# Kernel optimization log

Hardware: AMD Instinct MI355X
Metric: run time of the kernel (lower is better)

## Reference

```python
import jax, jax.numpy as jnp
import numpy as np


def setup_inputs() -> dict:
    key = jax.random.key(0)
    k1, k2, k3, k4 = jax.random.split(key, 4)
    b, c, h, w = 4, 256, 64, 64
    Fq_l = jax.random.normal(k1, (b, c, h, w), dtype=jnp.float32)
    Fp_l = jax.random.normal(k2, (b, c, h, w), dtype=jnp.float32)
    # 1x1 conv: weight [out=c//2, in=c], bias [c//2]
    W = jax.random.normal(k3, (c // 2, c), dtype=jnp.float32) * (1.0 / np.sqrt(c))
    bias = jax.random.normal(k4, (c // 2,), dtype=jnp.float32) * 0.01
    return {"Fq_l": Fq_l, "Fp_l": Fp_l, "W": W, "bias": bias}


def reference(Fq_l, Fp_l, W, bias):
    b, c, h, w = Fq_l.shape
    hw = h * w
    # 1x1 conv == per-pixel linear projection
    q = jnp.einsum('oc,bchw->bohw', W, Fq_l) + bias[None, :, None, None]
    p = jnp.einsum('oc,bchw->bohw', W, Fp_l) + bias[None, :, None, None]
    qf = q.reshape(b, -1, hw)  # [b, c/2, hw]
    pf = p.reshape(b, -1, hw)
    qf = qf / jnp.linalg.norm(qf, axis=1, keepdims=True)
    pf = pf / jnp.linalg.norm(pf, axis=1, keepdims=True)
    # cosine similarity, [b, hw, hw]
    sim = jnp.einsum('bcn,bcm->bnm', qf, pf)
    idx = jnp.argmax(sim, axis=-1)  # [b, hw]
    Fp_flat = Fp_l.reshape(b, c, hw)
    aligned = jnp.take_along_axis(Fp_flat, idx[:, None, :], axis=2)  # [b, c, hw]
    return aligned.reshape(b, c, h, w)
```

## Files before the change

### kernel.cpp

```cpp
#include <hip/hip_runtime.h>

#define HW 4096
#define BCAP 1024u
#define OCAP 65536u

typedef short bf16x8 __attribute__((ext_vector_type(8)));
typedef float f32x16 __attribute__((ext_vector_type(16)));

__device__ __forceinline__ ushort f2bf_rne(float f) {
    unsigned u = __float_as_uint(f);
    return (ushort)((u + 0x7FFFu + ((u >> 16) & 1u)) >> 16);
}

__global__ __launch_bounds__(256) void init_kernel(
    unsigned long long* __restrict__ best, unsigned* __restrict__ bcnt,
    unsigned* __restrict__ ocnt)
{
    int i = blockIdx.x * 256 + threadIdx.x;
    best[i] = 0ull;
    if (i < 512) bcnt[i] = 0u;
    if (i == 0) ocnt[0] = 0u;
}

__global__ __launch_bounds__(256) void transpose_w_kernel(
    const float* __restrict__ Wm, float* __restrict__ Wt)
{
    const int o = blockIdx.x;
    const int c = threadIdx.x;
    Wt[c * 128 + o] = Wm[o * 256 + c];
}

__global__ __launch_bounds__(256) void proj_kernel(
    const float* __restrict__ Fq, const float* __restrict__ Fp,
    const float* __restrict__ Wt, const float* __restrict__ bias,
    float* __restrict__ Qt, float* __restrict__ Pt,
    ushort* __restrict__ Qpk, ushort* __restrict__ Ppk,
    float* __restrict__ qnorm)
{
    __shared__ float Ws[64][128];
    __shared__ float Xs[64][64];
    __shared__ float psum[16][68];

    const int tid = threadIdx.x;
    const int z  = blockIdx.z;
    const float* __restrict__ X = z ? Fp : Fq;
    const int b  = blockIdx.y;
    const int n0 = blockIdx.x * 64;
    const int og = tid >> 4;
    const int ng = tid & 15;

    float acc[4][8];
    #pragma unroll
    for (int i = 0; i < 4; ++i)
        #pragma unroll
        for (int j = 0; j < 8; ++j) acc[i][j] = 0.f;

    for (int cc = 0; cc < 4; ++cc) {
        __syncthreads();
        {
            const float4* src = (const float4*)(Wt + (size_t)cc * 64 * 128);
            float4* dst = (float4*)Ws;
            #pragma unroll
            for (int it = 0; it < 8; ++it) dst[it * 256 + tid] = src[it * 256 + tid];
        }
        #pragma unroll
        for (int it = 0; it < 4; ++it) {
            int f = it * 256 + tid;
            int r = f >> 4, n4 = f & 15;
            *(float4*)&Xs[r][n4 * 4] =
                *(const float4*)&X[(size_t)(b * 256 + cc * 64 + r) * HW + n0 + n4 * 4];
        }
        __syncthreads();

        for (int r = 0; r < 64; ++r) {
            float4 w0 = *(const float4*)&Ws[r][og * 8];
            float4 w1 = *(const float4*)&Ws[r][og * 8 + 4];
            float4 xv = *(const float4*)&Xs[r][ng * 4];
            float wa[8] = {w0.x, w0.y, w0.z, w0.w, w1.x, w1.y, w1.z, w1.w};
            float xa[4] = {xv.x, xv.y, xv.z, xv.w};
            #pragma unroll
            for (int i = 0; i < 4; ++i)
                #pragma unroll
                for (int j = 0; j < 8; ++j)
                    acc[i][j] += wa[j] * xa[i];
        }
    }

    {
        float4 b0 = *(const float4*)&bias[og * 8];
        float4 b1 = *(const float4*)&bias[og * 8 + 4];
        float ba[8] = {b0.x, b0.y, b0.z, b0.w, b1.x, b1.y, b1.z, b1.w};
        #pragma unroll
        for (int i = 0; i < 4; ++i)
            #pragma unroll
            for (int j = 0; j < 8; ++j) acc[i][j] += ba[j];
    }

    #pragma unroll
    for (int i = 0; i < 4; ++i) {
        float s = 0.f;
        #pragma unroll
        for (int j = 0; j < 8; ++j) s += acc[i][j] * acc[i][j];
        psum[og][ng * 4 + i] = s;
    }
    __syncthreads();
    float tot[4];
    #pragma unroll
    for (int i = 0; i < 4; ++i) {
        float s = 0.f;
        #pragma unroll
        for (int g = 0; g < 16; ++g) s += psum[g][ng * 4 + i];
        tot[i] = s;
    }

    if (z) {
        #pragma unroll
        for (int i = 0; i < 4; ++i) {
            float s = 1.0f / sqrtf(tot[i]);
            #pragma unroll
            for (int j = 0; j < 8; ++j) acc[i][j] *= s;
        }
    } else if (og == 0) {
        #pragma unroll
        for (int i = 0; i < 4; ++i)
            qnorm[b * HW + n0 + ng * 4 + i] = sqrtf(tot[i]);
    }

    {
        float* __restrict__ T = z ? Pt : Qt;
        #pragma unroll
        for (int i = 0; i < 4; ++i) {
            size_t tb = ((size_t)b * HW + n0 + ng * 4 + i) * 128 + og * 8;
            *(float4*)&T[tb]     = make_float4(acc[i][0], acc[i][1], acc[i][2], acc[i][3]);
            *(float4*)&T[tb + 4] = make_float4(acc[i][4], acc[i][5], acc[i][6], acc[i][7]);
        }
    }
    {
        ushort* __restrict__ PK = z ? Ppk : Qpk;
        const int ks = og >> 1;
        #pragma unroll
        for (int i = 0; i < 4; ++i) {
            const int na  = n0 + ng * 4 + i;
            const int t32 = na >> 5;
            const int lt  = (na & 31) + 32 * (og & 1);
            ushort u[8];
            #pragma unroll
            for (int k = 0; k < 8; ++k) u[k] = f2bf_rne(acc[i][k]);
            size_t pk = ((((size_t)b * 128 + t32) * 8 + ks) * 64 + lt) * 8;
            uint4 w;
            w.x = (unsigned)u[0] | ((unsigned)u[1] << 16);
            w.y = (unsigned)u[2] | ((unsigned)u[3] << 16);
            w.z = (unsigned)u[4] | ((unsigned)u[5] << 16);
            w.w = (unsigned)u[6] | ((unsigned)u[7] << 16);
            *(uint4*)&PK[pk] = w;
        }
    }
}

__global__ __launch_bounds__(256, 2) void sim_max_kernel(
    const ushort* __restrict__ Qpk, const ushort* __restrict__ Ppk,
    float* __restrict__ Vmax)
{
    __shared__ ushort Qs[16384];
    __shared__ ushort Bs[16384];

    const int tid  = threadIdx.x;
    const int lane = tid & 63;
    const int w    = tid >> 6;
    const int nb   = blockIdx.x;
    const int b    = blockIdx.y;
    const int ms   = blockIdx.z;

    {
        const uint4* src = (const uint4*)(Qpk + ((size_t)b * 128 + nb * 4) * 4096);
        uint4* dst = (uint4*)Qs;
        #pragma unroll
        for (int it = 0; it < 8; ++it) dst[it * 256 + tid] = src[it * 256 + tid];
    }

    float bestv[16];
    #pragma unroll
    for (int r = 0; r < 16; ++r) bestv[r] = -1e30f;

    for (int ch = 0; ch < 8; ++ch) {
        __syncthreads();
        {
            const uint4* src = (const uint4*)(Ppk +
                ((size_t)b * 128 + ms * 32 + ch * 4) * 4096);
            uint4* dst = (uint4*)Bs;
            #pragma unroll
            for (int it = 0; it < 8; ++it) dst[it * 256 + tid] = src[it * 256 + tid];
        }
        __syncthreads();

        for (int mtl = 0; mtl < 4; ++mtl) {
            f32x16 acc;
            #pragma unroll
            for (int r = 0; r < 16; ++r) acc[r] = 0.f;
            #pragma unroll
            for (int ks = 0; ks < 8; ++ks) {
                bf16x8 a  = *(const bf16x8*)&Qs[((w   * 8 + ks) * 64 + lane) * 8];
                bf16x8 bb = *(const bf16x8*)&Bs[((mtl * 8 + ks) * 64 + lane) * 8];
                acc = __builtin_amdgcn_mfma_f32_32x32x16_bf16(a, bb, acc, 0, 0, 0);
            }
            #pragma unroll
            for (int r = 0; r < 16; ++r)
                bestv[r] = fmaxf(bestv[r], acc[r]);
        }
    }

    #pragma unroll
    for (int r = 0; r < 16; ++r) {
        float v = bestv[r];
        #pragma unroll
        for (int d = 1; d < 32; d <<= 1)
            v = fmaxf(v, __shfl_xor(v, d, 64));
        if ((lane & 31) == 0) {
            int nl_ = (r & 3) + 8 * (r >> 2) + 4 * (lane >> 5);
            int na = nb * 128 + w * 32 + nl_;
            Vmax[((size_t)b * HW + na) * 4 + ms] = v;
        }
    }
}

__global__ __launch_bounds__(256, 2) void sim_emit_kernel(
    const ushort* __restrict__ Qpk, const ushort* __restrict__ Ppk,
    const float* __restrict__ thr,
    unsigned* __restrict__ cand, unsigned* __restrict__ bcnt,
    unsigned* __restrict__ ocand, unsigned* __restrict__ ocnt)
{
    __shared__ ushort Qs[16384];
    __shared__ ushort Bs[16384];
    __shared__ unsigned lds_cand[BCAP];
    __shared__ unsigned lds_cnt;

    const int tid  = threadIdx.x;
    const int lane = tid & 63;
    const int w    = tid >> 6;
    const int nb   = blockIdx.x;
    const int b    = blockIdx.y;
    const int ms   = blockIdx.z;
    const int blk  = nb + 32 * (b + 4 * ms);

    if (tid == 0) lds_cnt = 0u;

    {
        const uint4* src = (const uint4*)(Qpk + ((size_t)b * 128 + nb * 4) * 4096);
        uint4* dst = (uint4*)Qs;
        #pragma unroll
        for (int it = 0; it < 8; ++it) dst[it * 256 + tid] = src[it * 256 + tid];
    }

    float thrreg[16];
    #pragma unroll
    for (int r = 0; r < 16; ++r) {
        int nl_ = (r & 3) + 8 * (r >> 2) + 4 * (lane >> 5);
        thrreg[r] = thr[b * HW + nb * 128 + w * 32 + nl_];
    }

    for (int ch = 0; ch < 8; ++ch) {
        __syncthreads();
        {
            const uint4* src = (const uint4*)(Ppk +
                ((size_t)b * 128 + ms * 32 + ch * 4) * 4096);
            uint4* dst = (uint4*)Bs;
            #pragma unroll
            for (int it = 0; it < 8; ++it) dst[it * 256 + tid] = src[it * 256 + tid];
        }
        __syncthreads();

        for (int mtl = 0; mtl < 4; ++mtl) {
            f32x16 acc;
            #pragma unroll
            for (int r = 0; r < 16; ++r) acc[r] = 0.f;
            #pragma unroll
            for (int ks = 0; ks < 8; ++ks) {
                bf16x8 a  = *(const bf16x8*)&Qs[((w   * 8 + ks) * 64 + lane) * 8];
                bf16x8 bb = *(const bf16x8*)&Bs[((mtl * 8 + ks) * 64 + lane) * 8];
                acc = __builtin_amdgcn_mfma_f32_32x32x16_bf16(a, bb, acc, 0, 0, 0);
            }

            const int m = ms * 1024 + ch * 128 + mtl * 32 + (lane & 31);
            #pragma unroll
            for (int r = 0; r < 16; ++r) {
                if (acc[r] >= thrreg[r]) {
                    int nl_ = (r & 3) + 8 * (r >> 2) + 4 * (lane >> 5);
                    int na = nb * 128 + w * 32 + nl_;
                    unsigned enc = ((unsigned)b << 24) | ((unsigned)na << 12) | (unsigned)m;
                    unsigned pos = atomicAdd(&lds_cnt, 1u);
                    if (pos < BCAP) {
                        lds_cand[pos] = enc;
                    } else {
                        unsigned op = atomicAdd(ocnt, 1u);
                        if (op < OCAP) ocand[op] = enc;
                    }
                }
            }
        }
    }

    __syncthreads();
    unsigned cnt = lds_cnt;
    if (cnt > BCAP) cnt = BCAP;
    for (unsigned i = tid; i < cnt; i += 256)
        cand[(size_t)blk * BCAP + i] = lds_cand[i];
    if (tid == 0) bcnt[blk] = cnt;
}

__global__ __launch_bounds__(256) void thresh_kernel(
    const float* __restrict__ Vmax, const float* __restrict__ qnorm,
    float* __restrict__ thr)
{
    int i = blockIdx.x * 256 + threadIdx.x;
    float g = -1e30f;
    #pragma unroll
    for (int s = 0; s < 4; ++s) g = fmaxf(g, Vmax[(size_t)i * 4 + s]);
    thr[i] = g - (0.016f * qnorm[i] + 1e-6f);
}

__device__ __forceinline__ void rescore_one(
    const float* __restrict__ Qt, const float* __restrict__ Pt,
    unsigned c, unsigned long long* __restrict__ best)
{
    int m = c & 0xFFF, n = (c >> 12) & 0xFFF, b = c >> 24;
    const float* __restrict__ q = Qt + ((size_t)b * HW + n) * 128;
    const float* __restrict__ p = Pt + ((size_t)b * HW + m) * 128;
    float acc = 0.f;
    for (int k = 0; k < 128; ++k) acc += q[k] * p[k];
    unsigned u = __float_as_uint(acc);
    unsigned kk = (u & 0x80000000u) ? ~u : (u | 0x80000000u);
    unsigned long long key = ((unsigned long long)kk << 32) | (unsigned)(4095 - m);
    atomicMax(&best[(size_t)b * HW + n], key);
}

__global__ __launch_bounds__(256) void rescore_kernel(
    const float* __restrict__ Qt, const float* __restrict__ Pt,
    const unsigned* __restrict__ cand, const unsigned* __restrict__ bcnt,
    const unsigned* __restrict__ ocand, const unsigned* __restrict__ ocnt,
    unsigned long long* __restrict__ best)
{
    const int blk = blockIdx.x;
    const int tid = threadIdx.x;
    unsigned cnt = bcnt[blk];
    for (unsigned i = tid; i < cnt; i += 256)
        rescore_one(Qt, Pt, cand[(size_t)blk * BCAP + i], best);

    unsigned total = ocnt[0];
    if (total > OCAP) total = OCAP;
    for (unsigned i = blk * 256 + tid; i < total; i += 512 * 256)
        rescore_one(Qt, Pt, ocand[i], best);
}

__global__ __launch_bounds__(256) void gather_kernel(
    const float* __restrict__ Fp, const unsigned long long* __restrict__ best,
    float* __restrict__ out)
{
    __shared__ float row[4096];
    const int blk = blockIdx.x;
    const int c = blk & 255;
    const int b = blk >> 8;
    const int tid = threadIdx.x;

    const float* __restrict__ src = Fp + ((size_t)b * 256 + c) * HW;
    #pragma unroll
    for (int it = 0; it < 4; ++it) {
        int f = it * 256 + tid;
        *(float4*)&row[f * 4] = *(const float4*)&src[f * 4];
    }
    __syncthreads();

    float* __restrict__ dst = out + ((size_t)b * 256 + c) * HW;
    #pragma unroll
    for (int it = 0; it < 16; ++it) {
        int n = it * 256 + tid;
        int m = 4095 - (int)(best[(size_t)b * HW + n] & 0xFFFull);
        dst[n] = row[m];
    }
}

extern "C" void kernel_launch(void* const* d_in, const int* in_sizes, int n_in,
                              void* d_out, int out_size, void* d_ws, size_t ws_size,
                              hipStream_t stream) {
    const float* Fq   = (const float*)d_in[0];
    const float* Fp   = (const float*)d_in[1];
    const float* Wm   = (const float*)d_in[2];
    const float* bias = (const float*)d_in[3];
    float* out = (float*)d_out;

    char* base = (char*)d_ws;
    float*  Qt    = (float*)(base);
    float*  Pt    = (float*)(base + (8u << 20));
    ushort* Qpk   = (ushort*)(base + (16u << 20));
    ushort* Ppk   = (ushort*)(base + (20u << 20));
    char* x = base + (24u << 20);
    float*  qnorm = (float*)x;              x += 65536;
    float*  Vmax  = (float*)x;              x += 262144;
    float*  thr   = (float*)x;              x += 65536;
    unsigned long long* best = (unsigned long long*)x; x += 131072;
    unsigned* bcnt = (unsigned*)x;          x += 4096;
    unsigned* ocnt = (unsigned*)x;          x += 16;
    unsigned* cand = (unsigned*)x;          x += (size_t)512 * BCAP * 4;
    unsigned* ocand = (unsigned*)x;         x += OCAP * 4;
    float*  Wtg   = (float*)x;

    init_kernel<<<64, 256, 0, stream>>>(best, bcnt, ocnt);
    transpose_w_kernel<<<128, 256, 0, stream>>>(Wm, Wtg);
    proj_kernel<<<dim3(64, 4, 2), 256, 0, stream>>>(Fq, Fp, Wtg, bias,
                                                    Qt, Pt, Qpk, Ppk, qnorm);
    sim_max_kernel<<<dim3(32, 4, 4), 256, 0, stream>>>(Qpk, Ppk, Vmax);
    thresh_kernel<<<64, 256, 0, stream>>>(Vmax, qnorm, thr);
    sim_emit_kernel<<<dim3(32, 4, 4), 256, 0, stream>>>(Qpk, Ppk, thr,
                                                        cand, bcnt, ocand, ocnt);
    rescore_kernel<<<512, 256, 0, stream>>>(Qt, Pt, cand, bcnt, ocand, ocnt, best);
    gather_kernel<<<1024, 256, 0, stream>>>(Fp, best, out);
}
```

Measured before the change: 176.0 us.

## Fuse two-pass similarity max/emit into single pass with running-max prefilter

Replaces the separate max pass, threshold kernel and emit pass with one similarity kernel. It keeps a running row max per chunk, pushes candidates within the margin of that running max into LDS, and refilters them against the block's final row max before writing them out. The init work is folded into the transpose and projection kernels, which removes two launches and halves the MFMA work. The risks are more early candidates spilling to the global overflow list, since the running max is looser early on. The per-block threshold now uses only the block's own max, not the global max across m-splits, so more candidates reach rescoring.

```diff
diff --git a/kernel.cpp b/kernel.cpp
--- a/kernel.cpp
+++ b/kernel.cpp
@@ -1,7 +1,8 @@
 #include <hip/hip_runtime.h>
 
 #define HW 4096
-#define BCAP 1024u
+#define PCAP 1536u
+#define FCAP 1024u
 #define OCAP 65536u
 
 typedef short bf16x8 __attribute__((ext_vector_type(8)));
@@ -12,22 +13,15 @@
     return (ushort)((u + 0x7FFFu + ((u >> 16) & 1u)) >> 16);
 }
 
-__global__ __launch_bounds__(256) void init_kernel(
-    unsigned long long* __restrict__ best, unsigned* __restrict__ bcnt,
-    unsigned* __restrict__ ocnt)
-{
-    int i = blockIdx.x * 256 + threadIdx.x;
-    best[i] = 0ull;
-    if (i < 512) bcnt[i] = 0u;
-    if (i == 0) ocnt[0] = 0u;
-}
-
 __global__ __launch_bounds__(256) void transpose_w_kernel(
-    const float* __restrict__ Wm, float* __restrict__ Wt)
+    const float* __restrict__ Wm, float* __restrict__ Wt,
+    unsigned* __restrict__ bcnt, unsigned* __restrict__ ocnt)
 {
     const int o = blockIdx.x;
     const int c = threadIdx.x;
     Wt[c * 128 + o] = Wm[o * 256 + c];
+    if (o < 2) bcnt[o * 256 + c] = 0u;
+    if (o == 2 && c == 0) ocnt[0] = 0u;
 }
 
 __global__ __launch_bounds__(256) void proj_kernel(
@@ -35,7 +29,7 @@
     const float* __restrict__ Wt, const float* __restrict__ bias,
     float* __restrict__ Qt, float* __restrict__ Pt,
     ushort* __restrict__ Qpk, ushort* __restrict__ Ppk,
-    float* __restrict__ qnorm)
+    float* __restrict__ qnorm, unsigned long long* __restrict__ best)
 {
     __shared__ float Ws[64][128];
     __shared__ float Xs[64][64];
@@ -120,10 +114,17 @@
             #pragma unroll
             for (int j = 0; j < 8; ++j) acc[i][j] *= s;
         }
-    } else if (og == 0) {
-        #pragma unroll
-        for (int i = 0; i < 4; ++i)
-            qnorm[b * HW + n0 + ng * 4 + i] = sqrtf(tot[i]);
+    } else {
+        if (og == 0) {
+            #pragma unroll
+            for (int i = 0; i < 4; ++i)
+                qnorm[b * HW + n0 + ng * 4 + i] = sqrtf(tot[i]);
+        }
+        if (og == 1) {
+            #pragma unroll
+            for (int i = 0; i < 4; ++i)
+                best[(size_t)b * HW + n0 + ng * 4 + i] = 0ull;
+        }
     }
 
     {
@@ -157,82 +158,19 @@
     }
 }
 
-__global__ __launch_bounds__(256, 2) void sim_max_kernel(
+__global__ __launch_bounds__(256, 2) void sim_kernel(
     const ushort* __restrict__ Qpk, const ushort* __restrict__ Ppk,
-    float* __restrict__ Vmax)
+    const float* __restrict__ qnorm,
+    unsigned* __restrict__ cand, unsigned* __restrict__ bcnt,
+    unsigned* __restrict__ ocand, unsigned* __restrict__ ocnt)
 {
     __shared__ ushort Qs[16384];
     __shared__ ushort Bs[16384];
-
-    const int tid  = threadIdx.x;
-    const int lane = tid & 63;
-    const int w    = tid >> 6;
-    const int nb   = blockIdx.x;
-    const int b    = blockIdx.y;
-    const int ms   = blockIdx.z;
-
-    {
-        const uint4* src = (const uint4*)(Qpk + ((size_t)b * 128 + nb * 4) * 4096);
-        uint4* dst = (uint4*)Qs;
-        #pragma unroll
-        for (int it = 0; it < 8; ++it) dst[it * 256 + tid] = src[it * 256 + tid];
-    }
-
-    float bestv[16];
-    #pragma unroll
-    for (int r = 0; r < 16; ++r) bestv[r] = -1e30f;
-
-    for (int ch = 0; ch < 8; ++ch) {
-        __syncthreads();
-        {
-            const uint4* src = (const uint4*)(Ppk +
-                ((size_t)b * 128 + ms * 32 + ch * 4) * 4096);
-            uint4* dst = (uint4*)Bs;
-            #pragma unroll
-            for (int it = 0; it < 8; ++it) dst[it * 256 + tid] = src[it * 256 + tid];
-        }
-        __syncthreads();
-
-        for (int mtl = 0; mtl < 4; ++mtl) {
-            f32x16 acc;
-            #pragma unroll
-            for (int r = 0; r < 16; ++r) acc[r] = 0.f;
-            #pragma unroll
-            for (int ks = 0; ks < 8; ++ks) {
-                bf16x8 a  = *(const bf16x8*)&Qs[((w   * 8 + ks) * 64 + lane) * 8];
-                bf16x8 bb = *(const bf16x8*)&Bs[((mtl * 8 + ks) * 64 + lane) * 8];
-                acc = __builtin_amdgcn_mfma_f32_32x32x16_bf16(a, bb, acc, 0, 0, 0);
-            }
-            #pragma unroll
-            for (int r = 0; r < 16; ++r)
-                bestv[r] = fmaxf(bestv[r], acc[r]);
-        }
-    }
-
-    #pragma unroll
-    for (int r = 0; r < 16; ++r) {
-        float v = bestv[r];
-        #pragma unroll
-        for (int d = 1; d < 32; d <<= 1)
-            v = fmaxf(v, __shfl_xor(v, d, 64));
-        if ((lane & 31) == 0) {
-            int nl_ = (r & 3) + 8 * (r >> 2) + 4 * (lane >> 5);
-            int na = nb * 128 + w * 32 + nl_;
-            Vmax[((size_t)b * HW + na) * 4 + ms] = v;
-        }
-    }
-}
-
-__global__ __launch_bounds__(256, 2) void sim_emit_kernel(
-    const ushort* __restrict__ Qpk, const ushort* __restrict__ Ppk,
-    const float* __restrict__ thr,
-    unsigned* __restrict__ cand, unsigned* __restrict__ bcnt,
-    unsigned* __restrict__ ocand, unsigned* __restrict__ ocnt)
-{
-    __shared__ ushort Qs[16384];
-    __shared__ ushort Bs[16384];
-    __shared__ unsigned lds_cand[BCAP];
-    __shared__ unsigned lds_cnt;
+    __shared__ unsigned pre_enc[PCAP];
+    __shared__ float    pre_val[PCAP];
+    __shared__ float rowmax[128];
+    __shared__ float margld[128];
+    __shared__ unsigned pre_cnt, fin_cnt;
 
     const int tid  = threadIdx.x;
     const int lane = tid & 63;
@@ -242,7 +180,7 @@
     const int ms   = blockIdx.z;
     const int blk  = nb + 32 * (b + 4 * ms);
 
-    if (tid == 0) lds_cnt = 0u;
+    if (tid == 0) { pre_cnt = 0u; fin_cnt = 0u; }
 
     {
         const uint4* src = (const uint4*)(Qpk + ((size_t)b * 128 + nb * 4) * 4096);
@@ -251,12 +189,16 @@
         for (int it = 0; it < 8; ++it) dst[it * 256 + tid] = src[it * 256 + tid];
     }
 
-    float thrreg[16];
+    float marg[16];
     #pragma unroll
     for (int r = 0; r < 16; ++r) {
         int nl_ = (r & 3) + 8 * (r >> 2) + 4 * (lane >> 5);
-        thrreg[r] = thr[b * HW + nb * 128 + w * 32 + nl_];
-    }
+        marg[r] = 0.016f * qnorm[b * HW + nb * 128 + w * 32 + nl_] + 1e-6f;
+    }
+
+    float bestv[16];
+    #pragma unroll
+    for (int r = 0; r < 16; ++r) bestv[r] = -1e30f;
 
     for (int ch = 0; ch < 8; ++ch) {
         __syncthreads();
@@ -269,27 +211,45 @@
         }
         __syncthreads();
 
+        bf16x8 af[8];
+        #pragma unroll
+        for (int ks = 0; ks < 8; ++ks)
+            af[ks] = *(const bf16x8*)&Qs[((w * 8 + ks) * 64 + lane) * 8];
+
+        f32x16 accbuf[4];
+        #pragma unroll
         for (int mtl = 0; mtl < 4; ++mtl) {
             f32x16 acc;
             #pragma unroll
             for (int r = 0; r < 16; ++r) acc[r] = 0.f;
             #pragma unroll
             for (int ks = 0; ks < 8; ++ks) {
-                bf16x8 a  = *(const bf16x8*)&Qs[((w   * 8 + ks) * 64 + lane) * 8];
                 bf16x8 bb = *(const bf16x8*)&Bs[((mtl * 8 + ks) * 64 + lane) * 8];
-                acc = __builtin_amdgcn_mfma_f32_32x32x16_bf16(a, bb, acc, 0, 0, 0);
+                acc = __builtin_amdgcn_mfma_f32_32x32x16_bf16(af[ks], bb, acc, 0, 0, 0);
             }
-
-            const int m = ms * 1024 + ch * 128 + mtl * 32 + (lane & 31);
-            #pragma unroll
-            for (int r = 0; r < 16; ++r) {
-                if (acc[r] >= thrreg[r]) {
-                    int nl_ = (r & 3) + 8 * (r >> 2) + 4 * (lane >> 5);
-                    int na = nb * 128 + w * 32 + nl_;
+            accbuf[mtl] = acc;
+        }
+
+        #pragma unroll
+        for (int r = 0; r < 16; ++r) {
+            float mx = fmaxf(fmaxf(accbuf[0][r], accbuf[1][r]),
+                             fmaxf(accbuf[2][r], accbuf[3][r]));
+            #pragma unroll
+            for (int d = 1; d < 32; d <<= 1)
+                mx = fmaxf(mx, __shfl_xor(mx, d, 64));
+            bestv[r] = fmaxf(bestv[r], mx);
+            const float th = mx - marg[r];
+            const int nl_ = (r & 3) + 8 * (r >> 2) + 4 * (lane >> 5);
+            const int na = nb * 128 + w * 32 + nl_;
+            #pragma unroll
+            for (int mtl = 0; mtl < 4; ++mtl) {
+                if (accbuf[mtl][r] >= th) {
+                    const int m = ms * 1024 + ch * 128 + mtl * 32 + (lane & 31);
                     unsigned enc = ((unsigned)b << 24) | ((unsigned)na << 12) | (unsigned)m;
-                    unsigned pos = atomicAdd(&lds_cnt, 1u);
-                    if (pos < BCAP) {
-                        lds_cand[pos] = enc;
+                    unsigned pos = atomicAdd(&pre_cnt, 1u);
+                    if (pos < PCAP) {
+                        pre_enc[pos] = enc;
+                        pre_val[pos] = accbuf[mtl][r];
                     } else {
                         unsigned op = atomicAdd(ocnt, 1u);
                         if (op < OCAP) ocand[op] = enc;
@@ -299,23 +259,33 @@
         }
     }
 
+    #pragma unroll
+    for (int r = 0; r < 16; ++r) {
+        if ((lane & 31) == 0) {
+            int nl_ = (r & 3) + 8 * (r >> 2) + 4 * (lane >> 5);
+            rowmax[w * 32 + nl_] = bestv[r];
+            margld[w * 32 + nl_] = marg[r];
+        }
+    }
     __syncthreads();
-    unsigned cnt = lds_cnt;
-    if (cnt > BCAP) cnt = BCAP;
-    for (unsigned i = tid; i < cnt; i += 256)
-        cand[(size_t)blk * BCAP + i] = lds_cand[i];
-    if (tid == 0) bcnt[blk] = cnt;
-}
-
-__global__ __launch_bounds__(256) void thresh_kernel(
-    const float* __restrict__ Vmax, const float* __restrict__ qnorm,
-    float* __restrict__ thr)
-{
-    int i = blockIdx.x * 256 + threadIdx.x;
-    float g = -1e30f;
-    #pragma unroll
-    for (int s = 0; s < 4; ++s) g = fmaxf(g, Vmax[(size_t)i * 4 + s]);
-    thr[i] = g - (0.016f * qnorm[i] + 1e-6f);
+
+    unsigned pcnt = pre_cnt < PCAP ? pre_cnt : PCAP;
+    for (unsigned i = tid; i < pcnt; i += 256) {
+        unsigned enc = pre_enc[i];
+        float v = pre_val[i];
+        int row = (enc >> 12) & 127;
+        if (v >= rowmax[row] - margld[row]) {
+            unsigned pos = atomicAdd(&fin_cnt, 1u);
+            if (pos < FCAP) {
+                cand[(size_t)blk * FCAP + pos] = enc;
+            } else {
+                unsigned op = atomicAdd(ocnt, 1u);
+                if (op < OCAP) ocand[op] = enc;
+            }
+        }
+    }
+    __syncthreads();
+    if (tid == 0) bcnt[blk] = fin_cnt < FCAP ? fin_cnt : FCAP;
 }
 
 __device__ __forceinline__ void rescore_one(
@@ -343,7 +313,7 @@
     const int tid = threadIdx.x;
     unsigned cnt = bcnt[blk];
     for (unsigned i = tid; i < cnt; i += 256)
-        rescore_one(Qt, Pt, cand[(size_t)blk * BCAP + i], best);
+        rescore_one(Qt, Pt, cand[(size_t)blk * FCAP + i], best);
 
     unsigned total = ocnt[0];
     if (total > OCAP) total = OCAP;
@@ -394,23 +364,18 @@
     ushort* Ppk   = (ushort*)(base + (20u << 20));
     char* x = base + (24u << 20);
     float*  qnorm = (float*)x;              x += 65536;
-    float*  Vmax  = (float*)x;              x += 262144;
-    float*  thr   = (float*)x;              x += 65536;
     unsigned long long* best = (unsigned long long*)x; x += 131072;
     unsigned* bcnt = (unsigned*)x;          x += 4096;
     unsigned* ocnt = (unsigned*)x;          x += 16;
-    unsigned* cand = (unsigned*)x;          x += (size_t)512 * BCAP * 4;
+    unsigned* cand = (unsigned*)x;          x += (size_t)512 * FCAP * 4;
     unsigned* ocand = (unsigned*)x;         x += OCAP * 4;
     float*  Wtg   = (float*)x;
 
-    init_kernel<<<64, 256, 0, stream>>>(best, bcnt, ocnt);
-    transpose_w_kernel<<<128, 256, 0, stream>>>(Wm, Wtg);
+    transpose_w_kernel<<<128, 256, 0, stream>>>(Wm, Wtg, bcnt, ocnt);
     proj_kernel<<<dim3(64, 4, 2), 256, 0, stream>>>(Fq, Fp, Wtg, bias,
-                                                    Qt, Pt, Qpk, Ppk, qnorm);
-    sim_max_kernel<<<dim3(32, 4, 4), 256, 0, stream>>>(Qpk, Ppk, Vmax);
-    thresh_kernel<<<64, 256, 0, stream>>>(Vmax, qnorm, thr);
-    sim_emit_kernel<<<dim3(32, 4, 4), 256, 0, stream>>>(Qpk, Ppk, thr,
-                                                        cand, bcnt, ocand, ocnt);
+                                                    Qt, Pt, Qpk, Ppk, qnorm, best);
+    sim_kernel<<<dim3(32, 4, 4), 256, 0, stream>>>(Qpk, Ppk, qnorm,
+                                                   cand, bcnt, ocand, ocnt);
     rescore_kernel<<<512, 256, 0, stream>>>(Qt, Pt, cand, bcnt, ocand, ocnt, best);
     gather_kernel<<<1024, 256, 0, stream>>>(Fp, best, out);
 }
```

Result: slower. 244.9 us (+39.1%).
